# Performance work log

Hardware: AMD Instinct MI355X
Metric: run time of the kernel (lower is better)

## Reference

```python
import jax, jax.numpy as jnp
import numpy as np

BETA = 0.25  # commitment loss weight (init kwarg)


def setup_inputs() -> dict:
    key = jax.random.key(0)
    k1, k2 = jax.random.split(key)
    z = jax.random.normal(k1, (16, 32, 32, 256), dtype=jnp.float32)
    embedding = jax.random.normal(k2, (8192, 256), dtype=jnp.float32)
    return {"z": z, "embedding": embedding}


def reference(z, embedding):
    # Eval-mode forward of EMAVectorQuantizer (EMA buffer update only runs in training).
    b, h, w, c = z.shape
    zf = z.reshape(-1, c)  # [N, d]
    # Squared L2 distance to every codebook entry: ||z||^2 + ||e||^2 - 2 z.e
    d = (jnp.sum(zf * zf, axis=1, keepdims=True)
         + jnp.sum(embedding * embedding, axis=1)
         - 2.0 * jnp.einsum('nd,kd->nk', zf, embedding))  # [N, n_embed]
    idx = jnp.argmin(d, axis=1)  # [N]
    z_q = embedding[idx].reshape(z.shape)  # codebook gather

    # Commitment loss (z_q is detached in the original)
    diff = BETA * jnp.mean((jax.lax.stop_gradient(z_q) - z) ** 2)

    # Straight-through estimator
    z_q = z + jax.lax.stop_gradient(z_q - z)
    z_q = jnp.transpose(z_q, (0, 3, 1, 2))  # b h w c -> b c h w

    # Perplexity as written in the source: each one-hot row contributes
    # exactly 1*log(1 + 1e-12), so the mean is a constant == exp(-log1p(1e-12)).
    perplexity = jnp.exp(-jnp.log1p(jnp.float32(1e-12)))

    return z_q, diff, idx, perplexity
```

## Files before the change

kernel.cpp:

```cpp
#include <hip/hip_runtime.h>
#include <hip/hip_bf16.h>
#include <hip/hip_fp16.h>

#define N_VEC   16384
#define K_CODES 8192
#define D_DIM   256
#define NSPLIT  8
#define KT_PER  16
#define BM      128

#define ZQ_SIZE  (16*256*32*32)
#define DIFF_OFF ZQ_SIZE
#define IDX_OFF  (ZQ_SIZE + 1)
#define PERP_OFF (ZQ_SIZE + 1 + N_VEC)

#define WS_ENORM 0
#define WS_ZH    65536
#define WS_EH    (WS_ZH + N_VEC * D_DIM * 2)
#define WS_P2    (WS_EH + K_CODES * D_DIM * 2)
#define WS_IDXI  (WS_P2 + NSPLIT * N_VEC * 16)
#define WS_LOSS  (WS_IDXI + N_VEC * 4)

typedef _Float16 f16x8 __attribute__((ext_vector_type(8)));
typedef float    f32x4 __attribute__((ext_vector_type(4)));

__device__ __forceinline__ unsigned long long skey(float s, int c) {
    unsigned u = __float_as_uint(s);
    u ^= (unsigned)((int)u >> 31) | 0x80000000u;
    return ((unsigned long long)u << 13) | (unsigned)c;
}

__device__ __forceinline__ int swz_off(int row, int dloc) {
    return row * 128 + ((((dloc >> 3) ^ (row & 7))) << 4) + ((dloc & 7) << 1);
}

__global__ __launch_bounds__(256) void convert_kernel(const float* __restrict__ Z,
                                                      const float* __restrict__ E,
                                                      char* __restrict__ ws) {
    const int t  = threadIdx.x;
    const int r  = blockIdx.x * 4 + (t >> 6);
    const int d0 = (t & 63) * 4;
    const float* src;
    char* dh;
    int rowl;
    const bool isE = (r >= N_VEC);
    if (!isE) {
        src  = Z + (size_t)r * D_DIM;
        rowl = r & 127;
        dh = ws + WS_ZH + (size_t)(((r >> 7) * 4) + (d0 >> 6)) * 16384;
    } else {
        const int re = r - N_VEC;
        src  = E + (size_t)re * D_DIM;
        rowl = re & 127;
        dh = ws + WS_EH + (size_t)(((re >> 7) * 4) + (d0 >> 6)) * 16384;
    }
    const float4 v = *reinterpret_cast<const float4*>(src + d0);
    const unsigned h0 = __half_as_ushort(__float2half(v.x));
    const unsigned h1 = __half_as_ushort(__float2half(v.y));
    const unsigned h2 = __half_as_ushort(__float2half(v.z));
    const unsigned h3 = __half_as_ushort(__float2half(v.w));
    uint2 hi;
    hi.x = h0 | (h1 << 16);  hi.y = h2 | (h3 << 16);
    *reinterpret_cast<uint2*>(dh + swz_off(rowl, d0 & 63)) = hi;

    if (isE) {
        float s = v.x * v.x + v.y * v.y + v.z * v.z + v.w * v.w;
        #pragma unroll
        for (int off = 32; off; off >>= 1) s += __shfl_down(s, off);
        if ((t & 63) == 0) ((float*)(ws + WS_ENORM))[r - N_VEC] = s;
    }
}

__global__ __launch_bounds__(256, 2) void vq_mfma_kernel(const char* __restrict__ ws_ro,
                                                         ulonglong2* __restrict__ part2) {
    __shared__ unsigned long long t2[512];

    const int tid  = threadIdx.x;
    const int lane = tid & 63, wid = tid >> 6;
    const int lane15 = lane & 15, g = lane >> 4;
    const int l7 = lane15 & 7;
    const int wm = wid >> 1, wn = wid & 1;
    const int bx = blockIdx.x, ksp = blockIdx.y;
    const int row0 = bx * BM;
    const int kbase = ksp * (K_CODES / NSPLIT);

    const char* zh = ws_ro + WS_ZH;
    const char* eh = ws_ro + WS_EH;
    const float* enorm = (const float*)(ws_ro + WS_ENORM);

    f16x8 a[4][2][4];
    {
        const char* tileA = zh + (size_t)(bx * 4) * 16384;
        #pragma unroll
        for (int dt = 0; dt < 4; ++dt)
            #pragma unroll
            for (int ks = 0; ks < 2; ++ks)
                #pragma unroll
                for (int m = 0; m < 4; ++m) {
                    const int row  = wm * 64 + m * 16 + lane15;
                    const int slot = (ks * 4 + g) ^ (row & 7);
                    a[dt][ks][m] = *reinterpret_cast<const f16x8*>(
                        tileA + (size_t)dt * 16384 + row * 128 + (slot << 4));
                }
    }

    int pb[2][2];
    #pragma unroll
    for (int ks = 0; ks < 2; ++ks)
        #pragma unroll
        for (int n = 0; n < 2; ++n)
            pb[ks][n] = (wn * 32 + n * 16 + lane15) * 128 + (((ks * 4 + g) ^ l7) << 4);

    float bestv[16];
    int   bestc[16];
    #pragma unroll
    for (int i = 0; i < 16; ++i) { bestv[i] = 3.0e38f; bestc[i] = 0; }

    const char* ebase = eh + (size_t)ksp * 524288;

    for (int kt = 0; kt < KT_PER; ++kt) {
        const int tb = (kt >> 1) * 65536 + (kt & 1) * 8192;

        f32x4 acc[4][2];
        #pragma unroll
        for (int m = 0; m < 4; ++m)
            #pragma unroll
            for (int n = 0; n < 2; ++n)
                #pragma unroll
                for (int q = 0; q < 4; ++q) acc[m][n][q] = 0.0f;

        #pragma unroll
        for (int dt = 0; dt < 4; ++dt) {
            f16x8 b[2][2];
            #pragma unroll
            for (int ks = 0; ks < 2; ++ks)
                #pragma unroll
                for (int n = 0; n < 2; ++n)
                    b[ks][n] = *reinterpret_cast<const f16x8*>(
                        ebase + tb + dt * 16384 + pb[ks][n]);
            #pragma unroll
            for (int ks = 0; ks < 2; ++ks)
                #pragma unroll
                for (int m = 0; m < 4; ++m)
                    #pragma unroll
                    for (int n = 0; n < 2; ++n)
                        acc[m][n] = __builtin_amdgcn_mfma_f32_16x16x32_f16(
                            a[dt][ks][m], b[ks][n], acc[m][n], 0, 0, 0);
        }

        const int kofs = kbase + kt * 64;
        const int c0 = kofs + wn * 32 + lane15;
        const int c1 = c0 + 16;
        const float en0 = enorm[c0];
        const float en1 = enorm[c1];
        #pragma unroll
        for (int m = 0; m < 4; ++m)
            #pragma unroll
            for (int q = 0; q < 4; ++q) {
                const int sl = m * 4 + q;
                const float s0 = fmaf(-2.0f, acc[m][0][q], en0);
                if (s0 < bestv[sl]) { bestv[sl] = s0; bestc[sl] = c0; }
                const float s1 = fmaf(-2.0f, acc[m][1][q], en1);
                if (s1 < bestv[sl]) { bestv[sl] = s1; bestc[sl] = c1; }
            }
    }

    #pragma unroll
    for (int sl = 0; sl < 16; ++sl) {
        const int m = sl >> 2, q = sl & 3;
        const unsigned long long k1 = skey(bestv[sl], bestc[sl]);
        unsigned long long m1 = k1;
        #pragma unroll
        for (int msk = 1; msk < 16; msk <<= 1) {
            const unsigned long long o = __shfl_xor(m1, msk);
            m1 = (o < m1) ? o : m1;
        }
        unsigned long long k2 = (k1 == m1) ? ~0ull : k1;
        #pragma unroll
        for (int msk = 1; msk < 16; msk <<= 1) {
            const unsigned long long o = __shfl_xor(k2, msk);
            k2 = (o < k2) ? o : k2;
        }
        if (lane15 == 0) {
            const int row64 = m * 16 + g * 4 + q;
            t2[(wid * 64 + row64) * 2 + 0] = m1;
            t2[(wid * 64 + row64) * 2 + 1] = k2;
        }
    }
    __syncthreads();
    if (tid < 128) {
        const int wm2 = tid >> 6, r64 = tid & 63;
        const unsigned long long a1 = t2[((wm2 * 2 + 0) * 64 + r64) * 2 + 0];
        const unsigned long long a2 = t2[((wm2 * 2 + 0) * 64 + r64) * 2 + 1];
        const unsigned long long b1 = t2[((wm2 * 2 + 1) * 64 + r64) * 2 + 0];
        const unsigned long long b2 = t2[((wm2 * 2 + 1) * 64 + r64) * 2 + 1];
        const unsigned long long r1 = (a1 < b1) ? a1 : b1;
        const unsigned long long hi = (a1 < b1) ? b1 : a1;
        const unsigned long long l2 = (a2 < b2) ? a2 : b2;
        const unsigned long long r2 = (hi < l2) ? hi : l2;
        ulonglong2 res;  res.x = r1;  res.y = r2;
        part2[(size_t)ksp * N_VEC + row0 + tid] = res;
    }
}

__global__ __launch_bounds__(256) void rescore_kernel(const float* __restrict__ Z,
                                                      const float* __restrict__ E,
                                                      const ulonglong2* __restrict__ part2,
                                                      int* __restrict__ idx_i,
                                                      float* __restrict__ out_idx,
                                                      float* __restrict__ lossp) {
    __shared__ double redl[4];
    const int tid = threadIdx.x, lane = tid & 63, wid = tid >> 6;
    const int r = blockIdx.x * 4 + wid;
    int c0 = 0, c1 = 0, c2 = 0, c3 = 0;
    if (lane == 0) {
        unsigned long long m0 = ~0ull, m1 = ~0ull, m2 = ~0ull, m3 = ~0ull;
        for (int s = 0; s < NSPLIT; ++s) {
            const ulonglong2 p = part2[(size_t)s * N_VEC + r];
            unsigned long long k = p.x;
            if (k < m0) { m3 = m2; m2 = m1; m1 = m0; m0 = k; }
            else if (k < m1) { m3 = m2; m2 = m1; m1 = k; }
            else if (k < m2) { m3 = m2; m2 = k; }
            else if (k < m3) { m3 = k; }
            k = p.y;
            if (k < m0) { m3 = m2; m2 = m1; m1 = m0; m0 = k; }
            else if (k < m1) { m3 = m2; m2 = m1; m1 = k; }
            else if (k < m2) { m3 = m2; m2 = k; }
            else if (k < m3) { m3 = k; }
        }
        c0 = (int)(m0 & 0x1FFFull);  c1 = (int)(m1 & 0x1FFFull);
        c2 = (int)(m2 & 0x1FFFull);  c3 = (int)(m3 & 0x1FFFull);
    }
    c0 = __shfl(c0, 0);  c1 = __shfl(c1, 0);
    c2 = __shfl(c2, 0);  c3 = __shfl(c3, 0);
    const float4 z4 = *reinterpret_cast<const float4*>(Z + (size_t)r * D_DIM + lane * 4);
    double d[4];
    const int cc[4] = {c0, c1, c2, c3};
    #pragma unroll
    for (int j = 0; j < 4; ++j) {
        const float4 e4 = *reinterpret_cast<const float4*>(E + (size_t)cc[j] * D_DIM + lane * 4);
        const double ax = (double)z4.x - (double)e4.x, ay = (double)z4.y - (double)e4.y;
        const double az = (double)z4.z - (double)e4.z, aw = (double)z4.w - (double)e4.w;
        d[j] = ax * ax + ay * ay + az * az + aw * aw;
    }
    #pragma unroll
    for (int off = 1; off < 64; off <<= 1) {
        #pragma unroll
        for (int j = 0; j < 4; ++j) d[j] += __shfl_xor(d[j], off);
    }
    if (lane == 0) {
        double bd = d[0];  int bi = c0;
        #pragma unroll
        for (int j = 1; j < 4; ++j) {
            if (d[j] < bd || (d[j] == bd && cc[j] < bi)) { bd = d[j]; bi = cc[j]; }
        }
        idx_i[r]   = bi;
        out_idx[r] = (float)bi;
        redl[wid]  = bd;
    }
    __syncthreads();
    if (tid == 0) lossp[blockIdx.x] = (float)(redl[0] + redl[1] + redl[2] + redl[3]);
}

__global__ __launch_bounds__(256) void gather_kernel(const float* __restrict__ E,
                                                     const int* __restrict__ idx_i,
                                                     float* __restrict__ out) {
    __shared__ float Ls[128 * 65];
    __shared__ int   sIdx[64];

    const int tid = threadIdx.x;
    const int gb  = blockIdx.x;
    const int n0  = gb * 64;
    const int b   = n0 >> 10;
    const int hwbase = n0 & 1023;

    if (tid < 64) sIdx[tid] = idx_i[n0 + tid];
    __syncthreads();

    for (int h = 0; h < 2; ++h) {
        if (h) __syncthreads();
        const int rowl = tid >> 2;
        const int qs   = tid & 3;
        const float* erow = E + (size_t)sIdx[rowl] * D_DIM + h * 128;
        #pragma unroll
        for (int m = 0; m < 8; ++m) {
            const int c4 = m * 4 + qs;
            const float4 v = *reinterpret_cast<const float4*>(erow + c4 * 4);
            Ls[(c4 * 4 + 0) * 65 + rowl] = v.x;
            Ls[(c4 * 4 + 1) * 65 + rowl] = v.y;
            Ls[(c4 * 4 + 2) * 65 + rowl] = v.z;
            Ls[(c4 * 4 + 3) * 65 + rowl] = v.w;
        }
        __syncthreads();
        const int wl   = tid & 63;
        const int csub = tid >> 6;
        #pragma unroll
        for (int pc = 0; pc < 32; ++pc) {
            const int c_l = pc * 4 + csub;
            const int c   = h * 128 + c_l;
            out[((size_t)(b * 256 + c)) * 1024 + hwbase + wl] = Ls[c_l * 65 + wl];
        }
    }
}

__global__ __launch_bounds__(256) void final_kernel(const float* __restrict__ lossp,
                                                    float* __restrict__ out) {
    __shared__ float red[4];
    const int tid = threadIdx.x;
    float s = 0.0f;
    for (int i = tid; i < N_VEC / 4; i += 256) s += lossp[i];
    #pragma unroll
    for (int off = 32; off; off >>= 1) s += __shfl_down(s, off);
    if ((tid & 63) == 0) red[tid >> 6] = s;
    __syncthreads();
    if (tid == 0) {
        const float total = red[0] + red[1] + red[2] + red[3];
        out[DIFF_OFF] = 0.25f * (total / (float)(N_VEC * D_DIM));
        out[PERP_OFF] = 1.0f;
    }
}

extern "C" void kernel_launch(void* const* d_in, const int* in_sizes, int n_in,
                              void* d_out, int out_size, void* d_ws, size_t ws_size,
                              hipStream_t stream) {
    const float* Z = (const float*)d_in[0];
    const float* E = (const float*)d_in[1];
    float* out = (float*)d_out;
    char*  ws  = (char*)d_ws;

    ulonglong2* part2   = (ulonglong2*)(ws + WS_P2);
    int*        idx_i   = (int*)(ws + WS_IDXI);
    float*      lossbuf = (float*)(ws + WS_LOSS);

    hipLaunchKernelGGL(convert_kernel, dim3((N_VEC + K_CODES) / 4), dim3(256), 0, stream, Z, E, ws);
    hipLaunchKernelGGL(vq_mfma_kernel, dim3(N_VEC / BM, NSPLIT), dim3(256), 0, stream,
                       (const char*)ws, part2);
    hipLaunchKernelGGL(rescore_kernel, dim3(N_VEC / 4), dim3(256), 0, stream,
                       Z, E, part2, idx_i, out + IDX_OFF, lossbuf);
    hipLaunchKernelGGL(gather_kernel, dim3(N_VEC / 64), dim3(256), 0, stream,
                       E, idx_i, out);
    hipLaunchKernelGGL(final_kernel, dim3(1), dim3(256), 0, stream, lossbuf, out);
}
```

Baseline: 132.1 us.

## Repartition warps to 32 rows x 64 codes and double-buffer codebook fragment loads

```diff
diff --git a/kernel.cpp b/kernel.cpp
--- a/kernel.cpp
+++ b/kernel.cpp
@@ -73,22 +73,19 @@
 
 __global__ __launch_bounds__(256, 2) void vq_mfma_kernel(const char* __restrict__ ws_ro,
                                                          ulonglong2* __restrict__ part2) {
-    __shared__ unsigned long long t2[512];
-
     const int tid  = threadIdx.x;
     const int lane = tid & 63, wid = tid >> 6;
     const int lane15 = lane & 15, g = lane >> 4;
     const int l7 = lane15 & 7;
-    const int wm = wid >> 1, wn = wid & 1;
     const int bx = blockIdx.x, ksp = blockIdx.y;
-    const int row0 = bx * BM;
+    const int row0w = bx * BM + wid * 32;
     const int kbase = ksp * (K_CODES / NSPLIT);
 
     const char* zh = ws_ro + WS_ZH;
     const char* eh = ws_ro + WS_EH;
     const float* enorm = (const float*)(ws_ro + WS_ENORM);
 
-    f16x8 a[4][2][4];
+    f16x8 a[4][2][2];
     {
         const char* tileA = zh + (size_t)(bx * 4) * 16384;
         #pragma unroll
@@ -96,77 +93,102 @@
             #pragma unroll
             for (int ks = 0; ks < 2; ++ks)
                 #pragma unroll
-                for (int m = 0; m < 4; ++m) {
-                    const int row  = wm * 64 + m * 16 + lane15;
+                for (int m = 0; m < 2; ++m) {
+                    const int row  = wid * 32 + m * 16 + lane15;
                     const int slot = (ks * 4 + g) ^ (row & 7);
                     a[dt][ks][m] = *reinterpret_cast<const f16x8*>(
                         tileA + (size_t)dt * 16384 + row * 128 + (slot << 4));
                 }
     }
-
-    int pb[2][2];
+    #pragma unroll
+    for (int dt = 0; dt < 4; ++dt)
+        #pragma unroll
+        for (int ks = 0; ks < 2; ++ks)
+            #pragma unroll
+            for (int m = 0; m < 2; ++m)
+                asm volatile("" : "+v"(a[dt][ks][m]));
+
+    int pb[2][4];
     #pragma unroll
     for (int ks = 0; ks < 2; ++ks)
         #pragma unroll
-        for (int n = 0; n < 2; ++n)
-            pb[ks][n] = (wn * 32 + n * 16 + lane15) * 128 + (((ks * 4 + g) ^ l7) << 4);
-
-    float bestv[16];
-    int   bestc[16];
-    #pragma unroll
-    for (int i = 0; i < 16; ++i) { bestv[i] = 3.0e38f; bestc[i] = 0; }
+        for (int n = 0; n < 4; ++n)
+            pb[ks][n] = (n * 16 + lane15) * 128 + (((ks * 4 + g) ^ l7) << 4);
 
     const char* ebase = eh + (size_t)ksp * 524288;
 
+    #define LOADB(dst, kt_, dt_)                                                       \
+    do {                                                                               \
+        const char* p_ = ebase + ((kt_) >> 1) * 65536 + ((kt_) & 1) * 8192             \
+                               + (dt_) * 16384;                                        \
+        _Pragma("unroll")                                                              \
+        for (int ks_ = 0; ks_ < 2; ++ks_)                                              \
+            _Pragma("unroll")                                                          \
+            for (int n_ = 0; n_ < 4; ++n_)                                             \
+                dst[ks_][n_] = *reinterpret_cast<const f16x8*>(p_ + pb[ks_][n_]);      \
+    } while (0)
+
+    #define MFMA_DT(dt_, bb)                                                           \
+    do {                                                                               \
+        _Pragma("unroll")                                                              \
+        for (int ks_ = 0; ks_ < 2; ++ks_)                                              \
+            _Pragma("unroll")                                                          \
+            for (int m_ = 0; m_ < 2; ++m_)                                             \
+                _Pragma("unroll")                                                      \
+                for (int n_ = 0; n_ < 4; ++n_)                                         \
+                    acc[m_][n_] = __builtin_amdgcn_mfma_f32_16x16x32_f16(              \
+                        a[dt_][ks_][m_], bb[ks_][n_], acc[m_][n_], 0, 0, 0);           \
+    } while (0)
+
+    float bestv[8];
+    int   bestc[8];
+    #pragma unroll
+    for (int i = 0; i < 8; ++i) { bestv[i] = 3.0e38f; bestc[i] = 0; }
+
+    f16x8 b0[2][4], b1[2][4];
+    LOADB(b0, 0, 0);
+
     for (int kt = 0; kt < KT_PER; ++kt) {
-        const int tb = (kt >> 1) * 65536 + (kt & 1) * 8192;
-
-        f32x4 acc[4][2];
-        #pragma unroll
-        for (int m = 0; m < 4; ++m)
+        const int kofs = kbase + kt * 64;
+        float en[4];
+        #pragma unroll
+        for (int n = 0; n < 4; ++n) en[n] = enorm[kofs + n * 16 + lane15];
+
+        f32x4 acc[2][4];
+        #pragma unroll
+        for (int m = 0; m < 2; ++m)
             #pragma unroll
-            for (int n = 0; n < 2; ++n)
+            for (int n = 0; n < 4; ++n)
                 #pragma unroll
                 for (int q = 0; q < 4; ++q) acc[m][n][q] = 0.0f;
 
-        #pragma unroll
-        for (int dt = 0; dt < 4; ++dt) {
-            f16x8 b[2][2];
+        LOADB(b1, kt, 1);
+        MFMA_DT(0, b0);
+        LOADB(b0, kt, 2);
+        MFMA_DT(1, b1);
+        LOADB(b1, kt, 3);
+        MFMA_DT(2, b0);
+        if (kt + 1 < KT_PER) LOADB(b0, kt + 1, 0);
+        MFMA_DT(3, b1);
+
+        #pragma unroll
+        for (int m = 0; m < 2; ++m)
             #pragma unroll
-            for (int ks = 0; ks < 2; ++ks)
+            for (int n = 0; n < 4; ++n) {
+                const int c = kofs + n * 16 + lane15;
                 #pragma unroll
-                for (int n = 0; n < 2; ++n)
-                    b[ks][n] = *reinterpret_cast<const f16x8*>(
-                        ebase + tb + dt * 16384 + pb[ks][n]);
-            #pragma unroll
-            for (int ks = 0; ks < 2; ++ks)
-                #pragma unroll
-                for (int m = 0; m < 4; ++m)
-                    #pragma unroll
-                    for (int n = 0; n < 2; ++n)
-                        acc[m][n] = __builtin_amdgcn_mfma_f32_16x16x32_f16(
-                            a[dt][ks][m], b[ks][n], acc[m][n], 0, 0, 0);
-        }
-
-        const int kofs = kbase + kt * 64;
-        const int c0 = kofs + wn * 32 + lane15;
-        const int c1 = c0 + 16;
-        const float en0 = enorm[c0];
-        const float en1 = enorm[c1];
-        #pragma unroll
-        for (int m = 0; m < 4; ++m)
-            #pragma unroll
-            for (int q = 0; q < 4; ++q) {
-                const int sl = m * 4 + q;
-                const float s0 = fmaf(-2.0f, acc[m][0][q], en0);
-                if (s0 < bestv[sl]) { bestv[sl] = s0; bestc[sl] = c0; }
-                const float s1 = fmaf(-2.0f, acc[m][1][q], en1);
-                if (s1 < bestv[sl]) { bestv[sl] = s1; bestc[sl] = c1; }
+                for (int q = 0; q < 4; ++q) {
+                    const int sl = m * 4 + q;
+                    const float s = fmaf(-2.0f, acc[m][n][q], en[n]);
+                    if (s < bestv[sl]) { bestv[sl] = s; bestc[sl] = c; }
+                }
             }
     }
-
-    #pragma unroll
-    for (int sl = 0; sl < 16; ++sl) {
+    #undef LOADB
+    #undef MFMA_DT
+
+    #pragma unroll
+    for (int sl = 0; sl < 8; ++sl) {
         const int m = sl >> 2, q = sl & 3;
         const unsigned long long k1 = skey(bestv[sl], bestc[sl]);
         unsigned long long m1 = k1;
@@ -182,24 +204,10 @@
             k2 = (o < k2) ? o : k2;
         }
         if (lane15 == 0) {
-            const int row64 = m * 16 + g * 4 + q;
-            t2[(wid * 64 + row64) * 2 + 0] = m1;
-            t2[(wid * 64 + row64) * 2 + 1] = k2;
-        }
-    }
-    __syncthreads();
-    if (tid < 128) {
-        const int wm2 = tid >> 6, r64 = tid & 63;
-        const unsigned long long a1 = t2[((wm2 * 2 + 0) * 64 + r64) * 2 + 0];
-        const unsigned long long a2 = t2[((wm2 * 2 + 0) * 64 + r64) * 2 + 1];
-        const unsigned long long b1 = t2[((wm2 * 2 + 1) * 64 + r64) * 2 + 0];
-        const unsigned long long b2 = t2[((wm2 * 2 + 1) * 64 + r64) * 2 + 1];
-        const unsigned long long r1 = (a1 < b1) ? a1 : b1;
-        const unsigned long long hi = (a1 < b1) ? b1 : a1;
-        const unsigned long long l2 = (a2 < b2) ? a2 : b2;
-        const unsigned long long r2 = (hi < l2) ? hi : l2;
-        ulonglong2 res;  res.x = r1;  res.y = r2;
-        part2[(size_t)ksp * N_VEC + row0 + tid] = res;
+            const int row = row0w + m * 16 + g * 4 + q;
+            ulonglong2 res;  res.x = m1;  res.y = k2;
+            part2[(size_t)ksp * N_VEC + row] = res;
+        }
     }
 }
 
```

Result: slower. 140.8 us (+6.6%).
